# Kernel optimization log

Hardware: AMD Instinct MI355X
Metric: run time of the kernel (lower is better)

## Reference

```python
import jax, jax.numpy as jnp
import numpy as np

# Fingertip landmark indices (end_ldmrk = [12,24,36,48,57] in flat coords -> landmarks {4,8,12,16,19})
_END_LANDMARKS = {4, 8, 12, 16, 19}

def _build_pairs():
    pairs = []
    for j in range(20):  # index in range(0, 60, 3) -> landmark j = index//3
        start = j + 1 if j in _END_LANDMARKS else j + 2  # skip adjacent landmark unless fingertip
        for k in range(start, 21):  # x in range(start, 63, 3) -> landmark k = x//3
            pairs.append((j, k))
    return np.asarray(pairs, dtype=np.int32)  # [195, 2]

_PAIRS = _build_pairs()
_I = jnp.asarray(_PAIRS[:, 0])  # [195]
_J = jnp.asarray(_PAIRS[:, 1])  # [195]


def setup_inputs() -> dict:
    key = jax.random.key(0)
    B = 1_000_000
    return {"tensor": jax.random.normal(key, (B, 63), dtype=jnp.float32)}


def reference(tensor):
    # tensor: [B, 63] = 21 landmarks x (x, y, z); distances use only x, y.
    B = tensor.shape[0]
    xy = tensor.reshape(B, 21, 3)[..., :2]          # [B, 21, 2]
    d = xy[:, _I, :] - xy[:, _J, :]                 # [B, 195, 2] only needed pairs
    feats = jnp.sqrt(jnp.sum(d * d, axis=-1))       # [B, 195] 2D Euclidean distances
    return jnp.concatenate([tensor, feats], axis=-1)  # [B, 258]
```

## Files before the change

kernel.cpp:

```cpp
#include <hip/hip_runtime.h>
#include <math.h>

#define ROWS 16
#define NPAIRS 195
#define NTHREADS 256
#define ROW_OUT 258
#define NLM 21
#define TILE_F (ROWS * ROW_OUT)
#define IN_F (ROWS * 63)
#define GRID 2048

typedef float f32x4 __attribute__((ext_vector_type(4)));

struct CodeTab { unsigned int c[NPAIRS]; };

constexpr CodeTab make_codes() {
    CodeTab t{};
    int n = 0;
    for (int a = 0; a < 20; ++a) {
        bool tip = (a == 4) || (a == 8) || (a == 12) || (a == 16) || (a == 19);
        int start = tip ? a + 1 : a + 2;
        for (int b = start; b < 21; ++b) {
            t.c[n] = (unsigned int)a | ((unsigned int)b << 16);
            ++n;
        }
    }
    return t;
}

__constant__ CodeTab CODES = make_codes();

__device__ __forceinline__ void scatter_tile(float* __restrict__ tile,
                                             float2* __restrict__ xy2,
                                             const float v[4], int r0, int col,
                                             int lm, int c3) {
#pragma unroll
    for (int e = 0; e < 4; ++e) {
        tile[(r0 + 4 * e) * ROW_OUT + col] = v[e];
    }
    if (c3 == 0) {
#pragma unroll
        for (int e = 0; e < 4; ++e) xy2[(r0 + 4 * e) * NLM + lm].x = v[e];
    } else if (c3 == 1) {
#pragma unroll
        for (int e = 0; e < 4; ++e) xy2[(r0 + 4 * e) * NLM + lm].y = v[e];
    }
}

__device__ __forceinline__ void compute_dists(float* __restrict__ tile,
                                              const float2* __restrict__ xy2,
                                              int t) {
    const int r = t >> 4;
    const int q = t & 15;
    const float2* __restrict__ xr = xy2 + r * NLM;
    float* __restrict__ drow = tile + r * ROW_OUT + 63;
#pragma unroll
    for (int k = 0; k < 13; ++k) {
        const int p = q + (k << 4);
        if (k < 12 || q < 3) {
            const unsigned int c = CODES.c[p];
            const float2 a = xr[c & 0xffu];
            const float2 b = xr[c >> 16];
            const float dx = a.x - b.x;
            const float dy = a.y - b.y;
            drow[p] = __builtin_amdgcn_sqrtf(dx * dx + dy * dy);
        }
    }
}

__global__ __launch_bounds__(NTHREADS, 8)
void HandKineticLayer_18545668784560_kernel(const float* __restrict__ in,
                                            float* __restrict__ out,
                                            int B) {
    __shared__ __align__(16) float tile[TILE_F];
    __shared__ float2 xy2[ROWS * NLM];

    const int t = threadIdx.x;
    const int ntiles = B / ROWS;

    const int r0 = t / 63;
    const int col = t - r0 * 63;
    const int lm = col / 3;
    const int c3 = col - lm * 3;

    const int tile0 = blockIdx.x;
    if (tile0 < ntiles) {
        if (t < 252) {
            const float* __restrict__ ip = in + (size_t)tile0 * IN_F + t;
            float v[4];
#pragma unroll
            for (int e = 0; e < 4; ++e)
                v[e] = __builtin_nontemporal_load(ip + 252 * e);
            scatter_tile(tile, xy2, v, r0, col, lm, c3);
        }
        __syncthreads();
    }

    for (int tl = tile0; tl < ntiles; tl += GRID) {
        const int nxt = tl + GRID;
        float vn[4] = {0.f, 0.f, 0.f, 0.f};
        const bool have_next = (nxt < ntiles) && (t < 252);
        if (have_next) {
            const float* __restrict__ ip = in + (size_t)nxt * IN_F + t;
#pragma unroll
            for (int e = 0; e < 4; ++e)
                vn[e] = __builtin_nontemporal_load(ip + 252 * e);
        }

        compute_dists(tile, xy2, t);
        __syncthreads();

        {
            const f32x4* __restrict__ tl4 =
                reinterpret_cast<const f32x4*>(&tile[0]);
            f32x4* __restrict__ o4 =
                reinterpret_cast<f32x4*>(out + (size_t)tl * TILE_F);
#pragma unroll
            for (int k = t; k < TILE_F / 4; k += NTHREADS) {
                __builtin_nontemporal_store(tl4[k], &o4[k]);
            }
        }
        __syncthreads();

        if (have_next) {
            scatter_tile(tile, xy2, vn, r0, col, lm, c3);
        }
        __syncthreads();
    }

    const int rem = B - ntiles * ROWS;
    if (rem > 0 && blockIdx.x == (unsigned)(ntiles % GRID)) {
        const int rowBase = ntiles * ROWS;
        const int nelem = rem * 63;
        for (int g = t; g < nelem; g += NTHREADS) {
            const float val = in[(size_t)rowBase * 63 + g];
            const int row = g / 63;
            const int cc = g - row * 63;
            tile[row * ROW_OUT + cc] = val;
            const int lmm = cc / 3;
            const int cc3 = cc - lmm * 3;
            if (cc3 == 0) xy2[row * NLM + lmm].x = val;
            else if (cc3 == 1) xy2[row * NLM + lmm].y = val;
        }
        __syncthreads();
        const int total = rem * NPAIRS;
        for (int idx = t; idx < total; idx += NTHREADS) {
            const int row = idx / NPAIRS;
            const int p = idx - row * NPAIRS;
            const unsigned int c = CODES.c[p];
            const float2 a = xy2[row * NLM + (int)(c & 0xffu)];
            const float2 b = xy2[row * NLM + (int)(c >> 16)];
            const float dx = a.x - b.x;
            const float dy = a.y - b.y;
            tile[row * ROW_OUT + 63 + p] = __builtin_amdgcn_sqrtf(dx * dx + dy * dy);
        }
        __syncthreads();
        const int nout = rem * ROW_OUT;
        for (int k = t; k < nout; k += NTHREADS) {
            out[(size_t)rowBase * ROW_OUT + k] = tile[k];
        }
    }
}

extern "C" void kernel_launch(void* const* d_in, const int* in_sizes, int n_in,
                              void* d_out, int out_size, void* d_ws, size_t ws_size,
                              hipStream_t stream) {
    const float* in = (const float*)d_in[0];
    float* out = (float*)d_out;
    const int B = in_sizes[0] / 63;
    hipLaunchKernelGGL(HandKineticLayer_18545668784560_kernel,
                       dim3(GRID), dim3(NTHREADS), 0, stream,
                       in, out, B);
}
```

Baseline: 256.9 us.

## Write outputs directly to global and double-buffer landmark xy in LDS

Removes the shared-memory output tile and its vectorized nontemporal copy-out. The 63 input columns and the 195 distances are now stored straight to global memory from registers. The xy landmark buffer is double-buffered, so each iteration needs one barrier instead of three. The cost is scalar, non-vectorized global stores (4-byte strided writes, no nontemporal hint), which may coalesce less efficiently than the earlier 16-byte row-contiguous stores.

Result: slower. 352.4 us (+37.2%).

```diff
diff --git a/kernel.cpp b/kernel.cpp
--- a/kernel.cpp
+++ b/kernel.cpp
@@ -9,8 +9,6 @@
 #define TILE_F (ROWS * ROW_OUT)
 #define IN_F (ROWS * 63)
 #define GRID 2048
-
-typedef float f32x4 __attribute__((ext_vector_type(4)));
 
 struct CodeTab { unsigned int c[NPAIRS]; };
 
@@ -30,14 +28,9 @@
 
 __constant__ CodeTab CODES = make_codes();
 
-__device__ __forceinline__ void scatter_tile(float* __restrict__ tile,
-                                             float2* __restrict__ xy2,
-                                             const float v[4], int r0, int col,
-                                             int lm, int c3) {
-#pragma unroll
-    for (int e = 0; e < 4; ++e) {
-        tile[(r0 + 4 * e) * ROW_OUT + col] = v[e];
-    }
+__device__ __forceinline__ void scatter_xy(float2* __restrict__ xy2,
+                                           const float v[4], int r0,
+                                           int lm, int c3) {
     if (c3 == 0) {
 #pragma unroll
         for (int e = 0; e < 4; ++e) xy2[(r0 + 4 * e) * NLM + lm].x = v[e];
@@ -47,33 +40,11 @@
     }
 }
 
-__device__ __forceinline__ void compute_dists(float* __restrict__ tile,
-                                              const float2* __restrict__ xy2,
-                                              int t) {
-    const int r = t >> 4;
-    const int q = t & 15;
-    const float2* __restrict__ xr = xy2 + r * NLM;
-    float* __restrict__ drow = tile + r * ROW_OUT + 63;
-#pragma unroll
-    for (int k = 0; k < 13; ++k) {
-        const int p = q + (k << 4);
-        if (k < 12 || q < 3) {
-            const unsigned int c = CODES.c[p];
-            const float2 a = xr[c & 0xffu];
-            const float2 b = xr[c >> 16];
-            const float dx = a.x - b.x;
-            const float dy = a.y - b.y;
-            drow[p] = __builtin_amdgcn_sqrtf(dx * dx + dy * dy);
-        }
-    }
-}
-
 __global__ __launch_bounds__(NTHREADS, 8)
 void HandKineticLayer_18545668784560_kernel(const float* __restrict__ in,
                                             float* __restrict__ out,
                                             int B) {
-    __shared__ __align__(16) float tile[TILE_F];
-    __shared__ float2 xy2[ROWS * NLM];
+    __shared__ float2 xy2[2][ROWS * NLM];
 
     const int t = threadIdx.x;
     const int ntiles = B / ROWS;
@@ -82,20 +53,23 @@
     const int col = t - r0 * 63;
     const int lm = col / 3;
     const int c3 = col - lm * 3;
+    const int rr = t >> 4;
+    const int q = t & 15;
 
     const int tile0 = blockIdx.x;
+    float v[4] = {0.f, 0.f, 0.f, 0.f};
     if (tile0 < ntiles) {
         if (t < 252) {
             const float* __restrict__ ip = in + (size_t)tile0 * IN_F + t;
-            float v[4];
 #pragma unroll
             for (int e = 0; e < 4; ++e)
                 v[e] = __builtin_nontemporal_load(ip + 252 * e);
-            scatter_tile(tile, xy2, v, r0, col, lm, c3);
+            scatter_xy(xy2[0], v, r0, lm, c3);
         }
         __syncthreads();
     }
 
+    int cur = 0;
     for (int tl = tile0; tl < ntiles; tl += GRID) {
         const int nxt = tl + GRID;
         float vn[4] = {0.f, 0.f, 0.f, 0.f};
@@ -107,25 +81,38 @@
                 vn[e] = __builtin_nontemporal_load(ip + 252 * e);
         }
 
-        compute_dists(tile, xy2, t);
-        __syncthreads();
+        if (t < 252) {
+            float* __restrict__ op = out + (size_t)tl * TILE_F
+                                         + (size_t)r0 * ROW_OUT + col;
+#pragma unroll
+            for (int e = 0; e < 4; ++e)
+                op[e * 4 * ROW_OUT] = v[e];
+        }
 
         {
-            const f32x4* __restrict__ tl4 =
-                reinterpret_cast<const f32x4*>(&tile[0]);
-            f32x4* __restrict__ o4 =
-                reinterpret_cast<f32x4*>(out + (size_t)tl * TILE_F);
+            const float2* __restrict__ xr = &xy2[cur][rr * NLM];
+            float* __restrict__ dg = out + (size_t)tl * TILE_F
+                                         + (size_t)rr * ROW_OUT + 63 + q;
 #pragma unroll
-            for (int k = t; k < TILE_F / 4; k += NTHREADS) {
-                __builtin_nontemporal_store(tl4[k], &o4[k]);
+            for (int k = 0; k < 13; ++k) {
+                if (k < 12 || q < 3) {
+                    const unsigned int c = CODES.c[q + (k << 4)];
+                    const float2 a = xr[c & 0xffu];
+                    const float2 b = xr[c >> 16];
+                    const float dx = a.x - b.x;
+                    const float dy = a.y - b.y;
+                    dg[k << 4] = __builtin_amdgcn_sqrtf(dx * dx + dy * dy);
+                }
             }
         }
-        __syncthreads();
 
         if (have_next) {
-            scatter_tile(tile, xy2, vn, r0, col, lm, c3);
+            scatter_xy(xy2[cur ^ 1], vn, r0, lm, c3);
         }
         __syncthreads();
+#pragma unroll
+        for (int e = 0; e < 4; ++e) v[e] = vn[e];
+        cur ^= 1;
     }
 
     const int rem = B - ntiles * ROWS;
@@ -136,11 +123,11 @@
             const float val = in[(size_t)rowBase * 63 + g];
             const int row = g / 63;
             const int cc = g - row * 63;
-            tile[row * ROW_OUT + cc] = val;
+            out[(size_t)(rowBase + row) * ROW_OUT + cc] = val;
             const int lmm = cc / 3;
             const int cc3 = cc - lmm * 3;
-            if (cc3 == 0) xy2[row * NLM + lmm].x = val;
-            else if (cc3 == 1) xy2[row * NLM + lmm].y = val;
+            if (cc3 == 0) xy2[0][row * NLM + lmm].x = val;
+            else if (cc3 == 1) xy2[0][row * NLM + lmm].y = val;
         }
         __syncthreads();
         const int total = rem * NPAIRS;
@@ -148,16 +135,12 @@
             const int row = idx / NPAIRS;
             const int p = idx - row * NPAIRS;
             const unsigned int c = CODES.c[p];
-            const float2 a = xy2[row * NLM + (int)(c & 0xffu)];
-            const float2 b = xy2[row * NLM + (int)(c >> 16)];
+            const float2 a = xy2[0][row * NLM + (int)(c & 0xffu)];
+            const float2 b = xy2[0][row * NLM + (int)(c >> 16)];
             const float dx = a.x - b.x;
             const float dy = a.y - b.y;
-            tile[row * ROW_OUT + 63 + p] = __builtin_amdgcn_sqrtf(dx * dx + dy * dy);
-        }
-        __syncthreads();
-        const int nout = rem * ROW_OUT;
-        for (int k = t; k < nout; k += NTHREADS) {
-            out[(size_t)rowBase * ROW_OUT + k] = tile[k];
+            out[(size_t)(rowBase + row) * ROW_OUT + 63 + p] =
+                __builtin_amdgcn_sqrtf(dx * dx + dy * dy);
         }
     }
 }
```
